# Optimization experiments

Hardware: AMD Instinct MI355X
Metric: run time of the kernel (lower is better)

## Reference

```python
import jax, jax.numpy as jnp
import numpy as np

NUM_EXPERTS = 64
HIDDEN_DIM = 4096
TOPK = 8


def setup_inputs() -> dict:
    key = jax.random.key(0)
    kx, kw = jax.random.split(key)
    x = jax.random.normal(kx, (16384, HIDDEN_DIM), dtype=jnp.float32)
    # nn.Linear weight is [num_experts, hidden_dim], init N(0, 0.01)
    W = jax.random.normal(kw, (NUM_EXPERTS, HIDDEN_DIM), dtype=jnp.float32) * 0.01
    return {"x": x, "W": W}


def reference(x, W):
    # router logits: [T, E]
    router_logits = jnp.einsum('th,eh->te', x, W)
    score = jnp.clip(router_logits, -2.0, 2.0)
    # top-k over experts (no router_bias branch)
    topk_scores, topk_indices = jax.lax.top_k(score, TOPK)  # [T, K]
    topk_probs = jax.nn.softmax(topk_scores, axis=-1)
    # dispatch index computation (counting-sort style)
    flat = topk_indices.reshape(-1)                      # [T*K]
    indices = jnp.argsort(flat, stable=True).astype(jnp.int32)
    tokens_per_expert = jnp.bincount(flat, length=NUM_EXPERTS)
    group_indices = jnp.cumsum(tokens_per_expert).astype(jnp.int32)
    tokens_per_expert_f = tokens_per_expert.astype(jnp.float32)
    # load-balance loss
    mean_tokens = tokens_per_expert_f / tokens_per_expert_f.sum()
    mean_prob = jax.nn.softmax(router_logits, axis=-1).mean(axis=0)
    lb_loss = jnp.dot(mean_tokens, mean_prob) * NUM_EXPERTS
    # z-loss
    zl = jnp.mean(jax.scipy.special.logsumexp(router_logits, axis=-1) ** 2)
    return (router_logits, topk_probs, topk_indices, group_indices,
            indices, tokens_per_expert, lb_loss, zl)
```

## Files before the change

### kernel.cpp

```cpp
#include <hip/hip_runtime.h>
#include <hip/hip_bf16.h>
#include <math.h>

#define NTOK   16384
#define NEXP   64
#define HID    4096
#define KSEL   8
#define EPS    7.5e-5f
#define NSPLIT 4
#define KSZ    (HID / NSPLIT)

typedef __attribute__((ext_vector_type(8))) short short8;
typedef __attribute__((ext_vector_type(4))) float f32x4;

#define O_LOGITS 0u
#define O_PROBS  1048576u
#define O_TIDX   1179648u
#define O_GROUP  1310720u
#define O_IDX    1310784u
#define O_TPE    1441856u
#define O_LB     1441920u
#define O_ZL     1441921u

#define W_LSQP    4096u
#define W_CBE     8192u
#define W_PREF    73728u
#define W_PSUM    262144u
#define W_FLAT    524288u
#define W_RNK     1048576u
#define W_WF      2097152u
#define W_PART    4194304u
#define PART_STRIDE 1048576ull

__device__ __forceinline__ unsigned short f2bf(float f) {
  unsigned u = __float_as_uint(f);
  return (unsigned short)((u + 0x7fffu + ((u >> 16) & 1u)) >> 16);
}

__device__ __forceinline__ void gload16(const void* g, void* l) {
  __builtin_amdgcn_global_load_lds((const __attribute__((address_space(1))) unsigned int*)g,
                                   (__attribute__((address_space(3))) unsigned int*)l, 16, 0, 0);
}

__global__ __launch_bounds__(256) void k_prep(const float* __restrict__ w,
                                              short8* __restrict__ wf) {
  const int kk   = blockIdx.x;
  const int nb   = threadIdx.x >> 6;
  const int lane = threadIdx.x & 63;
  const int n    = nb * 16 + (lane & 15);
  const int kb   = kk * 32 + (lane >> 4) * 8;
  const float4* wp = (const float4*)(w + (size_t)n * HID + kb);
  float4 f0 = wp[0], f1 = wp[1];
  float fv[8] = {f0.x, f0.y, f0.z, f0.w, f1.x, f1.y, f1.z, f1.w};
  short8 hi, lo;
#pragma unroll
  for (int j = 0; j < 8; ++j) {
    unsigned short h = f2bf(fv[j]);
    hi[j] = (short)h;
    float r = fv[j] - __uint_as_float((unsigned)h << 16);
    lo[j] = (short)f2bf(r);
  }
  size_t base = ((size_t)(kk * 4 + nb) * 2) * 64 + lane;
  wf[base] = hi;
  wf[base + 64] = lo;
}

__global__ __launch_bounds__(256, 4) void k_gemm(const float* __restrict__ x,
                                                 const short8* __restrict__ wf,
                                                 float* __restrict__ part) {
  __shared__ short8 wl[2][512];
  const int tid  = threadIdx.x;
  const int wv   = tid >> 6;
  const int lane = tid & 63;
  const int t0   = blockIdx.x * 64;
  const int k0   = blockIdx.y * KSZ;
  const int row  = t0 + wv * 16 + (lane & 15);

  const float* xp = x + (size_t)row * HID + k0 + (lane >> 4) * 8;
  const short8* wbase = wf + (size_t)(k0 >> 5) * 512;

  auto stage = [&](int c, int b) {
    const short8* src = wbase + (size_t)c * 512;
#pragma unroll
    for (int r = 0; r < 2; ++r) {
      const int o = r * 256 + wv * 64;
      gload16(src + o + lane, &wl[b][o]);
    }
  };

  f32x4 acc[4] = {{0,0,0,0},{0,0,0,0},{0,0,0,0},{0,0,0,0}};

  stage(0, 0);
  __syncthreads();
  const int nch = KSZ >> 5;
  for (int c = 0; c < nch; ++c) {
    const int b = c & 1;
    if (c + 1 < nch) stage(c + 1, b ^ 1);

    const float4* xq = (const float4*)(xp + c * 32);
    float4 f0 = xq[0], f1 = xq[1];
    unsigned xb[8] = {__float_as_uint(f0.x), __float_as_uint(f0.y),
                      __float_as_uint(f0.z), __float_as_uint(f0.w),
                      __float_as_uint(f1.x), __float_as_uint(f1.y),
                      __float_as_uint(f1.z), __float_as_uint(f1.w)};
    union { unsigned u[4]; short8 s; } ua, ul;
#pragma unroll
    for (int p = 0; p < 4; ++p) {
      unsigned b0 = xb[2 * p], b1 = xb[2 * p + 1];
      ua.u[p] = __builtin_amdgcn_perm(b1, b0, 0x07060302u);
      float r0 = __uint_as_float(b0) - __uint_as_float(b0 & 0xffff0000u);
      float r1 = __uint_as_float(b1) - __uint_as_float(b1 & 0xffff0000u);
      unsigned t0b = __float_as_uint(r0), t1b = __float_as_uint(r1);
      t0b += 0x7fffu + ((t0b >> 16) & 1u);
      t1b += 0x7fffu + ((t1b >> 16) & 1u);
      ul.u[p] = __builtin_amdgcn_perm(t1b, t0b, 0x07060302u);
    }
    short8 ah = ua.s, al = ul.s;

#pragma unroll
    for (int nb = 0; nb < 4; ++nb) {
      short8 bh = wl[b][nb * 128 + lane];
      short8 bl = wl[b][nb * 128 + 64 + lane];
      acc[nb] = __builtin_amdgcn_mfma_f32_16x16x32_bf16(ah, bh, acc[nb], 0, 0, 0);
      acc[nb] = __builtin_amdgcn_mfma_f32_16x16x32_bf16(al, bh, acc[nb], 0, 0, 0);
      acc[nb] = __builtin_amdgcn_mfma_f32_16x16x32_bf16(ah, bl, acc[nb], 0, 0, 0);
    }
    __syncthreads();
  }

  float* p = part + (size_t)blockIdx.y * PART_STRIDE;
  const int mrow = t0 + wv * 16 + (lane >> 4) * 4;
  const int col  = lane & 15;
#pragma unroll
  for (int nb = 0; nb < 4; ++nb)
#pragma unroll
    for (int r = 0; r < 4; ++r)
      p[(size_t)(mrow + r) * 64 + nb * 16 + col] = acc[nb][r];
}

__global__ __launch_bounds__(256) void k_reduce(const float* __restrict__ part,
                                                float* __restrict__ out_logits) {
  unsigned i4 = blockIdx.x * 256u + threadIdx.x;
  const float4* p4 = (const float4*)part;
  float4 v = p4[i4];
#pragma unroll
  for (int s = 1; s < NSPLIT; ++s) {
    float4 a = p4[(size_t)s * (PART_STRIDE / 4) + i4];
    v.x += a.x; v.y += a.y; v.z += a.z; v.w += a.w;
  }
  ((float4*)out_logits)[i4] = v;
}

__global__ __launch_bounds__(256) void k_rowwise(const float* __restrict__ lg,
                                                 const float* __restrict__ x,
                                                 const float* __restrict__ w,
                                                 float* __restrict__ out,
                                                 float* __restrict__ psum,
                                                 float* __restrict__ lsqp,
                                                 int* __restrict__ flat,
                                                 int* __restrict__ rnk_g,
                                                 int* __restrict__ cbe) {
  __shared__ float tile[64][68];
  __shared__ float rmv[64], invv[64], val8s[64];
  __shared__ unsigned long long Bmask[64];
  __shared__ int   fl_rows[64];
  __shared__ int   fl_n;
  __shared__ unsigned long long candmask;
  __shared__ double cexact[64];
  const int bid  = blockIdx.x;
  const int tid  = threadIdx.x;
  const int wv   = tid >> 6;
  const int lane = tid & 63;
  const int t0   = bid * 64;
  if (tid == 0) fl_n = 0;

  {
    const size_t boff = (size_t)bid * 4096;
#pragma unroll
    for (int k = 0; k < 16; ++k) {
      int idx = k * 256 + tid;
      tile[idx >> 6][idx & 63] = lg[boff + idx];
    }
  }
  __syncthreads();

  if (wv == 1) {
    const int r = lane;
    float rm = -3.0e38f;
#pragma unroll
    for (int c4 = 0; c4 < 16; ++c4) {
      float4 f = *(float4*)&tile[r][c4 * 4];
      rm = fmaxf(rm, fmaxf(fmaxf(f.x, f.y), fmaxf(f.z, f.w)));
    }
    float se = 0.0f;
#pragma unroll
    for (int c4 = 0; c4 < 16; ++c4) {
      float4 f = *(float4*)&tile[r][c4 * 4];
      se += expf(f.x - rm) + expf(f.y - rm) + expf(f.z - rm) + expf(f.w - rm);
    }
    rmv[r] = rm; invv[r] = 1.0f / se;
    float lse = rm + logf(se);
    float l2 = lse * lse;
#pragma unroll
    for (int o = 32; o > 0; o >>= 1) l2 += __shfl_down(l2, o);
    if (lane == 0) lsqp[bid] = l2;
  }
  __syncthreads();

  unsigned long long chosen = 0ull;
  int myidx[8];
  if (wv == 0) {
    const unsigned t = t0 + lane;
    float val[9]; int idx[9];
#pragma unroll
    for (int j = 0; j < 9; ++j) { val[j] = -3.0e38f; idx[j] = 0; }
    bool flag = false;
#pragma unroll
    for (int c4 = 0; c4 < 16; ++c4) {
      float4 f = *(float4*)&tile[lane][c4 * 4];
      float fe[4] = {f.x, f.y, f.z, f.w};
#pragma unroll
      for (int jj = 0; jj < 4; ++jj) {
        float v = fe[jj];
        flag = flag || (fabsf(fabsf(v) - 2.0f) < EPS);
        float c = fminf(fmaxf(v, -2.0f), 2.0f);
        int id = c4 * 4 + jj;
#pragma unroll
        for (int j = 0; j < 9; ++j) {
          bool sw = c > val[j];
          float tv = sw ? val[j] : c; int ti = sw ? idx[j] : id;
          val[j] = sw ? c : val[j];   idx[j] = sw ? id : idx[j];
          c = tv; id = ti;
        }
      }
    }
    val8s[lane] = val[8];
#pragma unroll
    for (int j = 0; j < 8; ++j) {
      float gap = val[j] - val[j + 1];
      bool bothclip = (val[j] == val[j + 1]) && (fabsf(val[j]) == 2.0f);
      flag = flag || (gap < EPS && !bothclip);
    }
    if (!flag) {
      float m = val[0], pe[8], sum = 0.0f;
#pragma unroll
      for (int j = 0; j < 8; ++j) { pe[j] = expf(val[j] - m); sum += pe[j]; }
      float inv = 1.0f / sum;
      *(float4*)&out[O_PROBS + (size_t)t * 8]     = make_float4(pe[0]*inv, pe[1]*inv, pe[2]*inv, pe[3]*inv);
      *(float4*)&out[O_PROBS + (size_t)t * 8 + 4] = make_float4(pe[4]*inv, pe[5]*inv, pe[6]*inv, pe[7]*inv);
      *(float4*)&out[O_TIDX + (size_t)t * 8]      = make_float4((float)idx[0], (float)idx[1], (float)idx[2], (float)idx[3]);
      *(float4*)&out[O_TIDX + (size_t)t * 8 + 4]  = make_float4((float)idx[4], (float)idx[5], (float)idx[6], (float)idx[7]);
      *(int4*)&flat[(size_t)t * 8]     = make_int4(idx[0], idx[1], idx[2], idx[3]);
      *(int4*)&flat[(size_t)t * 8 + 4] = make_int4(idx[4], idx[5], idx[6], idx[7]);
#pragma unroll
      for (int j = 0; j < 8; ++j) { myidx[j] = idx[j]; chosen |= 1ull << idx[j]; }
    } else {
      int sl = atomicAdd(&fl_n, 1);
      fl_rows[sl] = lane;
    }
  } else if (wv == 2 || wv == 3) {
    const int e = lane, half = wv - 2;
    float s = 0.0f;
#pragma unroll
    for (int r = 0; r < 32; ++r) {
      int rr = half * 32 + r;
      s += expf(tile[rr][e] - rmv[rr]) * invv[rr];
    }
    psum[(size_t)bid * 128 + half * 64 + e] = s;
  }
  __syncthreads();

  for (int i = 0; i < fl_n; ++i) {
    const int r = fl_rows[i];
    if (wv == 0) {
      float c = fminf(fmaxf(tile[r][lane], -2.0f), 2.0f);
      bool cnd = (c >= val8s[r] - 3.0f * EPS);
      unsigned long long m = __ballot(cnd);
      if (lane == 0) candmask = m;
    }
    __syncthreads();
    const unsigned long long m = candmask;
    const float* xr = x + (size_t)(t0 + r) * HID;
    {
      int ord = 0;
      for (int e = 0; e < 64; ++e) {
        if ((m >> e) & 1ull) {
          if ((ord & 3) == wv) {
            const float* wr = w + (size_t)e * HID;
            double p0 = 0.0, p1 = 0.0, p2 = 0.0, p3 = 0.0;
            const int kb = lane * 64;
            for (int k = kb; k < kb + 64; k += 4) {
              float4 xv = *(const float4*)&xr[k];
              float4 wv4 = *(const float4*)&wr[k];
              p0 = fma((double)xv.x, (double)wv4.x, p0);
              p1 = fma((double)xv.y, (double)wv4.y, p1);
              p2 = fma((double)xv.z, (double)wv4.z, p2);
              p3 = fma((double)xv.w, (double)wv4.w, p3);
            }
            double p = (p0 + p1) + (p2 + p3);
#pragma unroll
            for (int o = 32; o > 0; o >>= 1) p += __shfl_down(p, o);
            if (lane == 0) cexact[e] = fmin(fmax(p, -2.0), 2.0);
          }
          ord++;
        }
      }
    }
    __syncthreads();
    if (tid == r) {
      double val[8]; int idx[8];
#pragma unroll
      for (int j = 0; j < 8; ++j) { val[j] = -1.0e300; idx[j] = 0; }
      for (int e = 0; e < 64; ++e) {
        if (!((m >> e) & 1ull)) continue;
        double c = cexact[e];
        int id = e;
#pragma unroll
        for (int j = 0; j < 8; ++j) {
          bool sw = c > val[j];
          double tv = sw ? val[j] : c; int ti = sw ? idx[j] : id;
          val[j] = sw ? c : val[j];    idx[j] = sw ? id : idx[j];
          c = tv; id = ti;
        }
      }
      float mm = (float)val[0], pe[8], sum = 0.0f;
#pragma unroll
      for (int j = 0; j < 8; ++j) { pe[j] = expf((float)val[j] - mm); sum += pe[j]; }
      float inv = 1.0f / sum;
      const unsigned t = t0 + r;
      chosen = 0ull;
#pragma unroll
      for (int j = 0; j < 8; ++j) {
        out[O_PROBS + (size_t)t * 8 + j] = pe[j] * inv;
        out[O_TIDX  + (size_t)t * 8 + j] = (float)idx[j];
        flat[(size_t)t * 8 + j] = idx[j];
        myidx[j] = idx[j];
        chosen |= 1ull << idx[j];
      }
    }
    __syncthreads();
  }

  if (wv == 0) {
    for (int e = 0; e < 64; ++e) {
      unsigned long long b = __ballot((chosen >> e) & 1ull);
      if (lane == 0) Bmask[e] = b;
    }
    __builtin_amdgcn_wave_barrier();
    const unsigned long long below = (lane == 0) ? 0ull : (~0ull >> (64 - lane));
    int rr[8];
#pragma unroll
    for (int j = 0; j < 8; ++j)
      rr[j] = (int)__popcll(Bmask[myidx[j]] & below);
    *(int4*)&rnk_g[(size_t)bid * 512 + lane * 8]     = make_int4(rr[0], rr[1], rr[2], rr[3]);
    *(int4*)&rnk_g[(size_t)bid * 512 + lane * 8 + 4] = make_int4(rr[4], rr[5], rr[6], rr[7]);
    cbe[bid * 64 + lane] = (int)__popcll(Bmask[lane]);
  }
}

__global__ __launch_bounds__(256) void k_scan(const int* __restrict__ cbe,
                                              const float* __restrict__ psum,
                                              const float* __restrict__ lsqp,
                                              int* __restrict__ pref,
                                              float* __restrict__ out) {
  __shared__ int part4[4][64];
  __shared__ int segb[4][64];
  __shared__ int ctot[64];
  __shared__ float gsum[4][64];
  const int tid = threadIdx.x;
  const int e = tid & 63, g = tid >> 6;

  float ps = 0.0f;
  int cs = 0;
  for (int b = g * 64; b < g * 64 + 64; ++b) {
    ps += psum[(size_t)b * 128 + e] + psum[(size_t)b * 128 + 64 + e];
    cs += cbe[b * 64 + e];
  }
  gsum[g][e] = ps;
  part4[g][e] = cs;
  __syncthreads();

  if (tid < 64) {
    ctot[tid] = part4[0][tid] + part4[1][tid] + part4[2][tid] + part4[3][tid];
  }
  __syncthreads();

  if (tid < 64) {
    int incl = 0;
    for (int i = 0; i <= tid; ++i) incl += ctot[i];
    const int tpe = ctot[tid];
    out[O_TPE + tid]   = (float)tpe;
    out[O_GROUP + tid] = (float)incl;
    int base = incl - tpe;
    for (int gg = 0; gg < 4; ++gg) { segb[gg][tid] = base; base += part4[gg][tid]; }

    float pst = (gsum[0][tid] + gsum[1][tid]) + (gsum[2][tid] + gsum[3][tid]);
    float term = ((float)tpe / 131072.0f) * (pst / 16384.0f) * 64.0f;
#pragma unroll
    for (int o2 = 32; o2 > 0; o2 >>= 1) term += __shfl_down(term, o2);
    float zs = (lsqp[tid * 4] + lsqp[tid * 4 + 1]) + (lsqp[tid * 4 + 2] + lsqp[tid * 4 + 3]);
#pragma unroll
    for (int o2 = 32; o2 > 0; o2 >>= 1) zs += __shfl_down(zs, o2);
    if (tid == 0) { out[O_LB] = term; out[O_ZL] = zs / 16384.0f; }
  }
  __syncthreads();

  int run = segb[g][e];
  for (int b = g * 64; b < g * 64 + 64; ++b) {
    pref[b * 64 + e] = run;
    run += cbe[b * 64 + e];
  }
}

__global__ __launch_bounds__(256) void k_scatter(const int* __restrict__ flat,
                                                 const int* __restrict__ rnk,
                                                 const int* __restrict__ pref,
                                                 float* __restrict__ out) {
  const int j = blockIdx.x * 256 + threadIdx.x;
  const int e = flat[j];
  const int pos = pref[(j >> 9) * 64 + e] + rnk[j];
  out[O_IDX + pos] = (float)j;
}

extern "C" void kernel_launch(void* const* d_in, const int* in_sizes, int n_in,
                              void* d_out, int out_size, void* d_ws, size_t ws_size,
                              hipStream_t stream) {
  (void)in_sizes; (void)n_in; (void)out_size; (void)ws_size;
  const float* x  = (const float*)d_in[0];
  const float* Wm = (const float*)d_in[1];
  float* out = (float*)d_out;
  char*  ws  = (char*)d_ws;

  float*  lsqp   = (float*)(ws + W_LSQP);
  int*    cbe    = (int*)(ws + W_CBE);
  int*    pref   = (int*)(ws + W_PREF);
  float*  psum   = (float*)(ws + W_PSUM);
  int*    flat   = (int*)(ws + W_FLAT);
  int*    rnk    = (int*)(ws + W_RNK);
  short8* wf     = (short8*)(ws + W_WF);
  float*  part   = (float*)(ws + W_PART);

  k_prep   <<<dim3(128),  dim3(256), 0, stream>>>(Wm, wf);
  k_gemm   <<<dim3(NTOK / 64, NSPLIT), dim3(256), 0, stream>>>(x, wf, part);
  k_reduce <<<dim3(1024), dim3(256), 0, stream>>>(part, out + O_LOGITS);
  k_rowwise<<<dim3(256),  dim3(256), 0, stream>>>(out + O_LOGITS, x, Wm, out, psum, lsqp, flat, rnk, cbe);
  k_scan   <<<dim3(1),    dim3(256), 0, stream>>>(cbe, psum, lsqp, pref, out);
  k_scatter<<<dim3(512),  dim3(256), 0, stream>>>(flat, rnk, pref, out);
}
```

Before: 145.1 us.

## Halve rowwise block rows and parallelize expert scan across 64 blocks

The row-wise kernel now handles 32 tokens per block across 512 blocks instead of 64 tokens across 256, so more blocks are in flight. The single-block serial scan over per-block expert counts is replaced by a 64-block kernel, one block per expert, that does a wave-shuffle prefix scan. A tiny finalize kernel then computes the per-expert bases and the losses, and the scatter adds that base. The intent is to remove the serial one-block scan bottleneck and raise occupancy, at the cost of an extra kernel launch, half-idle waves in the row-wise kernel, and twice as many per-block count records.

```diff
diff --git a/kernel.cpp b/kernel.cpp
--- a/kernel.cpp
+++ b/kernel.cpp
@@ -9,6 +9,7 @@
 #define EPS    7.5e-5f
 #define NSPLIT 4
 #define KSZ    (HID / NSPLIT)
+#define RB     512
 
 typedef __attribute__((ext_vector_type(8))) short short8;
 typedef __attribute__((ext_vector_type(4))) float f32x4;
@@ -23,11 +24,14 @@
 #define O_ZL     1441921u
 
 #define W_LSQP    4096u
-#define W_CBE     8192u
-#define W_PREF    73728u
-#define W_PSUM    262144u
-#define W_FLAT    524288u
-#define W_RNK     1048576u
+#define W_TPE     8192u
+#define W_PST     12288u
+#define W_EBASE   16384u
+#define W_CBE     131072u
+#define W_PREF    393216u
+#define W_PSUM    655360u
+#define W_FLAT    1048576u
+#define W_RNK     1572864u
 #define W_WF      2097152u
 #define W_PART    4194304u
 #define PART_STRIDE 1048576ull
@@ -160,10 +164,10 @@
                                                  int* __restrict__ flat,
                                                  int* __restrict__ rnk_g,
                                                  int* __restrict__ cbe) {
-  __shared__ float tile[64][68];
-  __shared__ float rmv[64], invv[64], val8s[64];
+  __shared__ float tile[32][68];
+  __shared__ float rmv[32], invv[32], val8s[32];
   __shared__ unsigned long long Bmask[64];
-  __shared__ int   fl_rows[64];
+  __shared__ int   fl_rows[32];
   __shared__ int   fl_n;
   __shared__ unsigned long long candmask;
   __shared__ double cexact[64];
@@ -171,13 +175,13 @@
   const int tid  = threadIdx.x;
   const int wv   = tid >> 6;
   const int lane = tid & 63;
-  const int t0   = bid * 64;
+  const int t0   = bid * 32;
   if (tid == 0) fl_n = 0;
 
   {
-    const size_t boff = (size_t)bid * 4096;
-#pragma unroll
-    for (int k = 0; k < 16; ++k) {
+    const size_t boff = (size_t)bid * 2048;
+#pragma unroll
+    for (int k = 0; k < 8; ++k) {
       int idx = k * 256 + tid;
       tile[idx >> 6][idx & 63] = lg[boff + idx];
     }
@@ -185,22 +189,25 @@
   __syncthreads();
 
   if (wv == 1) {
-    const int r = lane;
-    float rm = -3.0e38f;
-#pragma unroll
-    for (int c4 = 0; c4 < 16; ++c4) {
-      float4 f = *(float4*)&tile[r][c4 * 4];
-      rm = fmaxf(rm, fmaxf(fmaxf(f.x, f.y), fmaxf(f.z, f.w)));
-    }
-    float se = 0.0f;
-#pragma unroll
-    for (int c4 = 0; c4 < 16; ++c4) {
-      float4 f = *(float4*)&tile[r][c4 * 4];
-      se += expf(f.x - rm) + expf(f.y - rm) + expf(f.z - rm) + expf(f.w - rm);
-    }
-    rmv[r] = rm; invv[r] = 1.0f / se;
-    float lse = rm + logf(se);
-    float l2 = lse * lse;
+    float l2 = 0.0f;
+    if (lane < 32) {
+      const int r = lane;
+      float rm = -3.0e38f;
+#pragma unroll
+      for (int c4 = 0; c4 < 16; ++c4) {
+        float4 f = *(float4*)&tile[r][c4 * 4];
+        rm = fmaxf(rm, fmaxf(fmaxf(f.x, f.y), fmaxf(f.z, f.w)));
+      }
+      float se = 0.0f;
+#pragma unroll
+      for (int c4 = 0; c4 < 16; ++c4) {
+        float4 f = *(float4*)&tile[r][c4 * 4];
+        se += expf(f.x - rm) + expf(f.y - rm) + expf(f.z - rm) + expf(f.w - rm);
+      }
+      rmv[r] = rm; invv[r] = 1.0f / se;
+      float lse = rm + logf(se);
+      l2 = lse * lse;
+    }
 #pragma unroll
     for (int o = 32; o > 0; o >>= 1) l2 += __shfl_down(l2, o);
     if (lane == 0) lsqp[bid] = l2;
@@ -208,8 +215,8 @@
   __syncthreads();
 
   unsigned long long chosen = 0ull;
-  int myidx[8];
-  if (wv == 0) {
+  int myidx[8] = {0,0,0,0,0,0,0,0};
+  if (wv == 0 && lane < 32) {
     const unsigned t = t0 + lane;
     float val[9]; int idx[9];
 #pragma unroll
@@ -262,8 +269,8 @@
     const int e = lane, half = wv - 2;
     float s = 0.0f;
 #pragma unroll
-    for (int r = 0; r < 32; ++r) {
-      int rr = half * 32 + r;
+    for (int r = 0; r < 16; ++r) {
+      int rr = half * 16 + r;
       s += expf(tile[rr][e] - rmv[rr]) * invv[rr];
     }
     psum[(size_t)bid * 128 + half * 64 + e] = s;
@@ -347,78 +354,98 @@
       if (lane == 0) Bmask[e] = b;
     }
     __builtin_amdgcn_wave_barrier();
-    const unsigned long long below = (lane == 0) ? 0ull : (~0ull >> (64 - lane));
-    int rr[8];
-#pragma unroll
-    for (int j = 0; j < 8; ++j)
-      rr[j] = (int)__popcll(Bmask[myidx[j]] & below);
-    *(int4*)&rnk_g[(size_t)bid * 512 + lane * 8]     = make_int4(rr[0], rr[1], rr[2], rr[3]);
-    *(int4*)&rnk_g[(size_t)bid * 512 + lane * 8 + 4] = make_int4(rr[4], rr[5], rr[6], rr[7]);
+    if (lane < 32) {
+      const unsigned long long below = (lane == 0) ? 0ull : (~0ull >> (64 - lane));
+      int rr[8];
+#pragma unroll
+      for (int j = 0; j < 8; ++j)
+        rr[j] = (int)__popcll(Bmask[myidx[j]] & below);
+      *(int4*)&rnk_g[(size_t)bid * 256 + lane * 8]     = make_int4(rr[0], rr[1], rr[2], rr[3]);
+      *(int4*)&rnk_g[(size_t)bid * 256 + lane * 8 + 4] = make_int4(rr[4], rr[5], rr[6], rr[7]);
+    }
     cbe[bid * 64 + lane] = (int)__popcll(Bmask[lane]);
   }
 }
 
 __global__ __launch_bounds__(256) void k_scan(const int* __restrict__ cbe,
                                               const float* __restrict__ psum,
-                                              const float* __restrict__ lsqp,
                                               int* __restrict__ pref,
-                                              float* __restrict__ out) {
-  __shared__ int part4[4][64];
-  __shared__ int segb[4][64];
-  __shared__ int ctot[64];
-  __shared__ float gsum[4][64];
+                                              int* __restrict__ tpe_g,
+                                              float* __restrict__ pst_g) {
+  __shared__ int   wsum[4];
+  __shared__ float fsum[4];
+  const int e = blockIdx.x;
   const int tid = threadIdx.x;
-  const int e = tid & 63, g = tid >> 6;
-
-  float ps = 0.0f;
-  int cs = 0;
-  for (int b = g * 64; b < g * 64 + 64; ++b) {
-    ps += psum[(size_t)b * 128 + e] + psum[(size_t)b * 128 + 64 + e];
-    cs += cbe[b * 64 + e];
-  }
-  gsum[g][e] = ps;
-  part4[g][e] = cs;
-  __syncthreads();
-
-  if (tid < 64) {
-    ctot[tid] = part4[0][tid] + part4[1][tid] + part4[2][tid] + part4[3][tid];
-  }
-  __syncthreads();
+  const int wv = tid >> 6, lane = tid & 63;
+
+  const int c0 = cbe[(2 * tid) * 64 + e];
+  const int c1 = cbe[(2 * tid + 1) * 64 + e];
+  const int s = c0 + c1;
+
+  int incl = s;
+#pragma unroll
+  for (int o = 1; o < 64; o <<= 1) {
+    int n = __shfl_up(incl, o);
+    if (lane >= o) incl += n;
+  }
+  if (lane == 63) wsum[wv] = incl;
+  __syncthreads();
+  int add = 0;
+#pragma unroll
+  for (int i = 0; i < 4; ++i) add += (i < wv) ? wsum[i] : 0;
+  incl += add;
+  const int excl = incl - s;
+  pref[(2 * tid) * 64 + e]     = excl;
+  pref[(2 * tid + 1) * 64 + e] = excl + c0;
+  if (tid == 255) tpe_g[e] = incl;
+
+  float p = psum[(size_t)(2 * tid) * 128 + e]     + psum[(size_t)(2 * tid) * 128 + 64 + e]
+          + psum[(size_t)(2 * tid + 1) * 128 + e] + psum[(size_t)(2 * tid + 1) * 128 + 64 + e];
+#pragma unroll
+  for (int o = 32; o > 0; o >>= 1) p += __shfl_down(p, o);
+  if (lane == 0) fsum[wv] = p;
+  __syncthreads();
+  if (tid == 0) pst_g[e] = (fsum[0] + fsum[1]) + (fsum[2] + fsum[3]);
+}
+
+__global__ __launch_bounds__(256) void k_fin(const int* __restrict__ tpe_g,
+                                             const float* __restrict__ pst_g,
+                                             const float* __restrict__ lsqp,
+                                             int* __restrict__ ebase,
+                                             float* __restrict__ out) {
+  __shared__ float zbuf[4];
+  const int tid = threadIdx.x;
+  const int wv = tid >> 6, lane = tid & 63;
+
+  float z = lsqp[tid] + lsqp[256 + tid];
+#pragma unroll
+  for (int o = 32; o > 0; o >>= 1) z += __shfl_down(z, o);
+  if (lane == 0) zbuf[wv] = z;
+  __syncthreads();
+  if (tid == 0) out[O_ZL] = ((zbuf[0] + zbuf[1]) + (zbuf[2] + zbuf[3])) / 16384.0f;
 
   if (tid < 64) {
     int incl = 0;
-    for (int i = 0; i <= tid; ++i) incl += ctot[i];
-    const int tpe = ctot[tid];
+    for (int i = 0; i <= tid; ++i) incl += tpe_g[i];
+    const int tpe = tpe_g[tid];
     out[O_TPE + tid]   = (float)tpe;
     out[O_GROUP + tid] = (float)incl;
-    int base = incl - tpe;
-    for (int gg = 0; gg < 4; ++gg) { segb[gg][tid] = base; base += part4[gg][tid]; }
-
-    float pst = (gsum[0][tid] + gsum[1][tid]) + (gsum[2][tid] + gsum[3][tid]);
-    float term = ((float)tpe / 131072.0f) * (pst / 16384.0f) * 64.0f;
-#pragma unroll
-    for (int o2 = 32; o2 > 0; o2 >>= 1) term += __shfl_down(term, o2);
-    float zs = (lsqp[tid * 4] + lsqp[tid * 4 + 1]) + (lsqp[tid * 4 + 2] + lsqp[tid * 4 + 3]);
-#pragma unroll
-    for (int o2 = 32; o2 > 0; o2 >>= 1) zs += __shfl_down(zs, o2);
-    if (tid == 0) { out[O_LB] = term; out[O_ZL] = zs / 16384.0f; }
-  }
-  __syncthreads();
-
-  int run = segb[g][e];
-  for (int b = g * 64; b < g * 64 + 64; ++b) {
-    pref[b * 64 + e] = run;
-    run += cbe[b * 64 + e];
+    ebase[tid] = incl - tpe;
+    float term = ((float)tpe / 131072.0f) * (pst_g[tid] / 16384.0f) * 64.0f;
+#pragma unroll
+    for (int o = 32; o > 0; o >>= 1) term += __shfl_down(term, o);
+    if (tid == 0) out[O_LB] = term;
   }
 }
 
 __global__ __launch_bounds__(256) void k_scatter(const int* __restrict__ flat,
                                                  const int* __restrict__ rnk,
                                                  const int* __restrict__ pref,
+                                                 const int* __restrict__ ebase,
                                                  float* __restrict__ out) {
   const int j = blockIdx.x * 256 + threadIdx.x;
   const int e = flat[j];
-  const int pos = pref[(j >> 9) * 64 + e] + rnk[j];
+  const int pos = ebase[e] + pref[(j >> 8) * 64 + e] + rnk[j];
   out[O_IDX + pos] = (float)j;
 }
 
@@ -432,6 +459,9 @@
   char*  ws  = (char*)d_ws;
 
   float*  lsqp   = (float*)(ws + W_LSQP);
+  int*    tpe_g  = (int*)(ws + W_TPE);
+  float*  pst_g  = (float*)(ws + W_PST);
+  int*    ebase  = (int*)(ws + W_EBASE);
   int*    cbe    = (int*)(ws + W_CBE);
   int*    pref   = (int*)(ws + W_PREF);
   float*  psum   = (float*)(ws + W_PSUM);
@@ -443,7 +473,8 @@
   k_prep   <<<dim3(128),  dim3(256), 0, stream>>>(Wm, wf);
   k_gemm   <<<dim3(NTOK / 64, NSPLIT), dim3(256), 0, stream>>>(x, wf, part);
   k_reduce <<<dim3(1024), dim3(256), 0, stream>>>(part, out + O_LOGITS);
-  k_rowwise<<<dim3(256),  dim3(256), 0, stream>>>(out + O_LOGITS, x, Wm, out, psum, lsqp, flat, rnk, cbe);
-  k_scan   <<<dim3(1),    dim3(256), 0, stream>>>(cbe, psum, lsqp, pref, out);
-  k_scatter<<<dim3(512),  dim3(256), 0, stream>>>(flat, rnk, pref, out);
-}
+  k_rowwise<<<dim3(RB),   dim3(256), 0, stream>>>(out + O_LOGITS, x, Wm, out, psum, lsqp, flat, rnk, cbe);
+  k_scan   <<<dim3(64),   dim3(256), 0, stream>>>(cbe, psum, pref, tpe_g, pst_g);
+  k_fin    <<<dim3(1),    dim3(256), 0, stream>>>(tpe_g, pst_g, lsqp, ebase, out);
+  k_scatter<<<dim3(512),  dim3(256), 0, stream>>>(flat, rnk, pref, ebase, out);
+}
```

Result: slower. 151.5 us (+4.4%).
